# Optimization experiments

Measured on AMD Instinct MI355X. Metric: run time of the kernel, lower is better.

The kernel has to match this reference:

```python
import jax, jax.numpy as jnp
import numpy as np

DIM = 1024
HEADS = 16


def setup_inputs() -> dict:
    key = jax.random.key(0)
    k1, k2, k3, k4 = jax.random.split(key, 4)
    X = jax.random.normal(k1, (4, 2048, DIM), dtype=jnp.float32)
    # torch Linear weight is [out, in]; store transposed [in, out] for x @ W
    W_qkv = jax.random.normal(k2, (DIM, 3 * DIM), dtype=jnp.float32) * (DIM ** -0.5)
    W_out = jax.random.normal(k3, (DIM, DIM), dtype=jnp.float32) * (DIM ** -0.5)
    b_out = jax.random.normal(k4, (DIM,), dtype=jnp.float32) * 0.01
    return {"X": X, "W_qkv": W_qkv, "W_out": W_out, "b_out": b_out}


def reference(X, W_qkv, W_out, b_out):
    b, t, d = X.shape
    h = HEADS
    hd = d // h
    scale = d ** -0.5  # NOTE: scales by full dim, matching the original module
    qkv = X @ W_qkv  # [b, t, 3d]
    q, k, v = jnp.split(qkv, 3, axis=-1)
    # [b, t, d] -> [b, h, t, hd]
    def to_heads(x):
        return x.reshape(b, t, h, hd).transpose(0, 2, 1, 3)
    q, k, v = to_heads(q), to_heads(k), to_heads(v)
    dots = jnp.einsum('bhid,bhjd->bhij', q, k) * scale  # [b, h, t, t]
    attn = jax.nn.softmax(dots, axis=-1)
    out = jnp.einsum('bhij,bhjd->bhid', attn, v)  # [b, h, t, hd]
    out = out.transpose(0, 2, 1, 3).reshape(b, t, d)
    return out @ W_out + b_out
```

## Files before the change

### kernel.cpp

```cpp
#include <hip/hip_runtime.h>
#include <hip/hip_bf16.h>
#include <stdint.h>

#define DIMD 1024
#define NB 4
#define NT 2048
#define NH 16
#define BT (NB*NT)
#define NQKV (3*DIMD)

typedef __attribute__((ext_vector_type(8))) __bf16 bf16x8;
typedef __attribute__((ext_vector_type(4))) __bf16 bf16x4;
typedef __attribute__((ext_vector_type(4))) float f32x4;
typedef __attribute__((ext_vector_type(16))) float f32x16;

#define MFMA16(a,b,c) __builtin_amdgcn_mfma_f32_16x16x32_bf16((a),(b),(c),0,0,0)
#define MFMA32(a,b,c) __builtin_amdgcn_mfma_f32_32x32x16_bf16((a),(b),(c),0,0,0)

#define QSCALE 0.0450842200277801f

__device__ __forceinline__ void gld16(const void* g, void* l) {
  __builtin_amdgcn_global_load_lds((const __attribute__((address_space(1))) void*)g,
                                   (__attribute__((address_space(3))) void*)l,
                                   16, 0, 0);
}

__device__ __forceinline__ unsigned pkbf(float a, float b) {
  unsigned short ua = __builtin_bit_cast(unsigned short, (__bf16)a);
  unsigned short ub = __builtin_bit_cast(unsigned short, (__bf16)b);
  return (unsigned)ua | ((unsigned)ub << 16);
}

__global__ __launch_bounds__(256) void k_cvt(const float* __restrict__ in,
                                             __bf16* __restrict__ out, int n4) {
  int i = blockIdx.x * blockDim.x + threadIdx.x;
  int st = gridDim.x * blockDim.x;
  for (; i < n4; i += st) {
    float4 v = ((const float4*)in)[i];
    bf16x4 o;
    o[0] = (__bf16)v.x; o[1] = (__bf16)v.y; o[2] = (__bf16)v.z; o[3] = (__bf16)v.w;
    ((bf16x4*)out)[i] = o;
  }
}

__global__ __launch_bounds__(256) void k_tcvt(const float* __restrict__ in,
                                              __bf16* __restrict__ out, int K, int N) {
  __shared__ __bf16 t[64][72];
  int n0 = blockIdx.x * 64, k0 = blockIdx.y * 64;
  int r = threadIdx.x >> 2, c0 = (threadIdx.x & 3) * 16;
  const float4* src = (const float4*)(in + (size_t)(k0 + r) * N + n0 + c0);
#pragma unroll
  for (int i = 0; i < 4; ++i) {
    float4 v = src[i];
    t[r][c0 + i*4 + 0] = (__bf16)v.x;
    t[r][c0 + i*4 + 1] = (__bf16)v.y;
    t[r][c0 + i*4 + 2] = (__bf16)v.z;
    t[r][c0 + i*4 + 3] = (__bf16)v.w;
  }
  __syncthreads();
  bf16x8 o0, o1;
#pragma unroll
  for (int i = 0; i < 8; ++i) o0[i] = t[c0 + i][r];
#pragma unroll
  for (int i = 0; i < 8; ++i) o1[i] = t[c0 + 8 + i][r];
  __bf16* dst = out + (size_t)(n0 + r) * K + k0 + c0;
  *(bf16x8*)dst = o0;
  *(bf16x8*)(dst + 8) = o1;
}

template<int MODE>
__global__ __launch_bounds__(512, 1) void k_gemm256(const __bf16* __restrict__ A,
                                                    const __bf16* __restrict__ Bt,
                                                    int nbx,
                                                    __bf16* __restrict__ oQK,
                                                    __bf16* __restrict__ oVt,
                                                    float* __restrict__ oF,
                                                    const float* __restrict__ bias) {
  constexpr int KK = 1024, KT = 32;
  __shared__ alignas(16) char L[98304];
  const int tid = threadIdx.x;
  const int lane = tid & 63, wid = tid >> 6;
  const int lr = lane & 15, lo = lane >> 4;
  const int wm = wid >> 2, wn = wid & 3;
  const int cpx = gridDim.x >> 3;
  const int swz = (blockIdx.x & 7) * cpx + (blockIdx.x >> 3);
  const int bx = swz % nbx, by = swz / nbx;
  const int m0 = by * 128, n0 = bx * 256;

  const int srow = tid >> 2, sk = (tid & 3) * 8;
  const __bf16* Asr = A + (size_t)(m0 + srow) * KK + sk;
  const __bf16* Bs0 = Bt + (size_t)(n0 + srow) * KK + sk;
  const __bf16* Bs1 = Bt + (size_t)(n0 + 128 + srow) * KK + sk;

  auto STAGE = [&](int t) {
    const int s = t & 3;
    char* dA = L + s * 8192 + tid * 16;
    char* dB = L + 32768 + s * 16384 + tid * 16;
    gld16(Asr + t * 32, dA);
    gld16(Bs0 + t * 32, dB);
    gld16(Bs1 + t * 32, dB + 8192);
  };

  const __bf16* fA = (const __bf16*)L + (size_t)(wm * 64 + lr) * 32 + lo * 8;
  const __bf16* fB = (const __bf16*)(L + 32768) + (size_t)(wn * 64 + lr) * 32 + lo * 8;

  f32x4 acc[4][4] = {};
  STAGE(0); STAGE(1); STAGE(2);

  for (int t = 0; t < KT; ++t) {
    if (t < KT - 2)       asm volatile("s_waitcnt vmcnt(6)" ::: "memory");
    else if (t == KT - 2) asm volatile("s_waitcnt vmcnt(3)" ::: "memory");
    else                  asm volatile("s_waitcnt vmcnt(0)" ::: "memory");
    asm volatile("s_barrier" ::: "memory");
    if (t + 3 < KT) STAGE(t + 3);
    const __bf16* fa = fA + (t & 3) * 4096;
    const __bf16* fb = fB + (t & 3) * 8192;
    bf16x8 Af[4], Bf[4];
#pragma unroll
    for (int i = 0; i < 4; ++i) Af[i] = *(const bf16x8*)(fa + i * 512);
#pragma unroll
    for (int j = 0; j < 4; ++j) Bf[j] = *(const bf16x8*)(fb + j * 512);
    __builtin_amdgcn_s_setprio(1);
#pragma unroll
    for (int i = 0; i < 4; ++i)
#pragma unroll
      for (int j = 0; j < 4; ++j)
        acc[i][j] = MFMA16(Af[i], Bf[j], acc[i][j]);
    __builtin_amdgcn_s_setprio(0);
  }

  const int mb = m0 + wm * 64 + lo * 4;
  if (MODE == 0) {
    if (n0 < 1024) {
#pragma unroll
      for (int i = 0; i < 4; ++i)
#pragma unroll
        for (int j = 0; j < 4; ++j) {
          int col = n0 + wn * 64 + j * 16 + lr;
          int row = mb + i * 16;
#pragma unroll
          for (int r = 0; r < 4; ++r)
            oQK[(size_t)(row + r) * 2048 + col] = (__bf16)(acc[i][j][r] * QSCALE);
        }
    } else if (n0 < 2048) {
#pragma unroll
      for (int i = 0; i < 4; ++i)
#pragma unroll
        for (int j = 0; j < 4; ++j) {
          int col = n0 + wn * 64 + j * 16 + lr;
          int row = mb + i * 16;
#pragma unroll
          for (int r = 0; r < 4; ++r)
            oQK[(size_t)(row + r) * 2048 + col] = (__bf16)acc[i][j][r];
        }
    } else {
#pragma unroll
      for (int i = 0; i < 4; ++i)
#pragma unroll
        for (int j = 0; j < 4; ++j) {
          int dd = n0 - 2048 + wn * 64 + j * 16 + lr;
          int row = mb + i * 16;
          int bb = row >> 11, tt = row & 2047;
          bf16x4 pk;
#pragma unroll
          for (int r = 0; r < 4; ++r) pk[r] = (__bf16)acc[i][j][r];
          *(bf16x4*)(oVt + ((size_t)(bb << 10) + dd) * 2048 + tt) = pk;
        }
    }
  } else {
#pragma unroll
    for (int i = 0; i < 4; ++i)
#pragma unroll
      for (int j = 0; j < 4; ++j) {
        int col = n0 + wn * 64 + j * 16 + lr;
        float bv = bias[col];
        int row = mb + i * 16;
#pragma unroll
        for (int r = 0; r < 4; ++r)
          oF[(size_t)(row + r) * 1024 + col] = acc[i][j][r] + bv;
      }
  }
}

__global__ __launch_bounds__(256, 2) void k_attn(const __bf16* __restrict__ QK,
                                                 const __bf16* __restrict__ Vt,
                                                 __bf16* __restrict__ AO) {
  __shared__ alignas(16) __bf16 Ks[2][64 * 72];
  __shared__ alignas(16) __bf16 Vs[2][64 * 72];
  const int tid = threadIdx.x, w = tid >> 6, lane = tid & 63;
  const int l31 = lane & 31, hi = lane >> 5;
  const int P = blockIdx.x;
  const int low3 = P & 7, g = P >> 3;
  const int qc = g & 7;
  const int bh = ((g >> 3) << 3) + low3;
  const int h = bh & 15, b = bh >> 4;
  const int q0 = qc * 256 + w * 64;

  bf16x8 qfA[4], qfB[4];
  {
    const __bf16* Qb = QK + (size_t)(b * 2048 + q0 + l31) * 2048 + h * 64 + hi * 8;
#pragma unroll
    for (int dc = 0; dc < 4; ++dc) qfA[dc] = *(const bf16x8*)(Qb + dc * 16);
    Qb += (size_t)32 * 2048;
#pragma unroll
    for (int dc = 0; dc < 4; ++dc) qfB[dc] = *(const bf16x8*)(Qb + dc * 16);
  }
  const __bf16* Kg = QK + (size_t)(b * 2048) * 2048 + 1024 + h * 64;
  const __bf16* Vg = Vt + (size_t)(b * 1024 + h * 64) * 2048;

  const int i0 = tid, i1 = 256 + tid, i2 = 512 + tid;
  int r0 = i0 / 9, c0 = i0 - r0 * 9; c0 = (c0 == 8) ? 0 : c0;
  int r1 = i1 / 9, c1 = i1 - r1 * 9; c1 = (c1 == 8) ? 0 : c1;
  int r2 = i2 / 9, c2 = i2 - r2 * 9; c2 = (c2 == 8) ? 0 : c2;
  const __bf16* kP0 = Kg + (size_t)r0 * 2048 + c0 * 8;
  const __bf16* kP1 = Kg + (size_t)r1 * 2048 + c1 * 8;
  const __bf16* kP2 = Kg + (size_t)r2 * 2048 + c2 * 8;
  const __bf16* vP0 = Vg + (size_t)r0 * 2048 + c0 * 8;
  const __bf16* vP1 = Vg + (size_t)r1 * 2048 + c1 * 8;
  const __bf16* vP2 = Vg + (size_t)r2 * 2048 + c2 * 8;

  f32x16 oA0 = {0,0,0,0,0,0,0,0,0,0,0,0,0,0,0,0};
  f32x16 oA1 = {0,0,0,0,0,0,0,0,0,0,0,0,0,0,0,0};
  f32x16 oB0 = {0,0,0,0,0,0,0,0,0,0,0,0,0,0,0,0};
  f32x16 oB1 = {0,0,0,0,0,0,0,0,0,0,0,0,0,0,0,0};
  float lnA = 0.f, lnB = 0.f;

  auto STAGE = [&](int x) {
    char* bK = (char*)&Ks[x][0];
    char* bV = (char*)&Vs[x][0];
    gld16(kP0, bK + i0 * 16);
    gld16(vP0, bV + i0 * 16);
    gld16(kP1, bK + i1 * 16);
    gld16(vP1, bV + i1 * 16);
    if (tid < 64) {
      gld16(kP2, bK + i2 * 16);
      gld16(vP2, bV + i2 * 16);
    }
    kP0 += 64 * 2048; kP1 += 64 * 2048; kP2 += 64 * 2048;
    vP0 += 64; vP1 += 64; vP2 += 64;
  };

  auto SMPACK = [&](const f32x16& s0, const f32x16& s1, unsigned pw[4][4], float& ln) {
    float p0a[16], p1a[16];
#pragma unroll
    for (int r = 0; r < 16; ++r) {
      p0a[r] = __builtin_amdgcn_exp2f(s0[r]);
      p1a[r] = __builtin_amdgcn_exp2f(s1[r]);
    }
    float sA = 0.f, sB = 0.f, sC = 0.f, sD = 0.f;
#pragma unroll
    for (int r = 0; r < 4; ++r) {
      sA += p0a[r];      sB += p0a[4 + r];
      sC += p0a[8 + r];  sD += p0a[12 + r];
      sA += p1a[r];      sB += p1a[4 + r];
      sC += p1a[8 + r];  sD += p1a[12 + r];
    }
    ln += (sA + sB) + (sC + sD);
#pragma unroll
    for (int c = 0; c < 4; ++c) {
      const float* pp = (c < 2) ? p0a : p1a;
      const int rb = (c & 1) * 8;
      unsigned A01 = pkbf(pp[rb + 0], pp[rb + 1]);
      unsigned A23 = pkbf(pp[rb + 2], pp[rb + 3]);
      unsigned A45 = pkbf(pp[rb + 4], pp[rb + 5]);
      unsigned A67 = pkbf(pp[rb + 6], pp[rb + 7]);
      asm("v_permlane32_swap_b32 %0, %1" : "+v"(A01), "+v"(A45));
      asm("v_permlane32_swap_b32 %0, %1" : "+v"(A23), "+v"(A67));
      pw[c][0] = A01; pw[c][1] = A23; pw[c][2] = A45; pw[c][3] = A67;
    }
  };

  STAGE(0);
  asm volatile("s_waitcnt vmcnt(0)" ::: "memory");
  __syncthreads();

  int x = 0;
#pragma unroll 2
  for (int t = 0; t < 32; ++t) {
    if (t < 31) STAGE(x ^ 1);
    const __bf16* Kl = &Ks[x][0];
    const __bf16* Vl = &Vs[x][0];

    f32x16 sA0 = {0,0,0,0,0,0,0,0,0,0,0,0,0,0,0,0};
    f32x16 sA1 = {0,0,0,0,0,0,0,0,0,0,0,0,0,0,0,0};
    f32x16 sB0 = {0,0,0,0,0,0,0,0,0,0,0,0,0,0,0,0};
    f32x16 sB1 = {0,0,0,0,0,0,0,0,0,0,0,0,0,0,0,0};
    {
      bf16x8 kf[8];
#pragma unroll
      for (int dc = 0; dc < 4; ++dc)
        kf[dc] = *(const bf16x8*)(Kl + l31 * 72 + dc * 16 + hi * 8);
#pragma unroll
      for (int dc = 0; dc < 4; ++dc)
        kf[4 + dc] = *(const bf16x8*)(Kl + (32 + l31) * 72 + dc * 16 + hi * 8);
      __builtin_amdgcn_s_setprio(1);
#pragma unroll
      for (int dc = 0; dc < 4; ++dc) {
        sA0 = MFMA32(kf[dc], qfA[dc], sA0);
        sB0 = MFMA32(kf[dc], qfB[dc], sB0);
        sA1 = MFMA32(kf[4 + dc], qfA[dc], sA1);
        sB1 = MFMA32(kf[4 + dc], qfB[dc], sB1);
      }
      __builtin_amdgcn_s_setprio(0);
    }

    unsigned pwA[4][4], pwB[4][4];
    SMPACK(sA0, sA1, pwA, lnA);
    SMPACK(sB0, sB1, pwB, lnB);

    {
      bf16x8 vf[8];
#pragma unroll
      for (int c = 0; c < 4; ++c)
        vf[c] = *(const bf16x8*)(Vl + l31 * 72 + c * 16 + hi * 8);
#pragma unroll
      for (int c = 0; c < 4; ++c)
        vf[4 + c] = *(const bf16x8*)(Vl + (32 + l31) * 72 + c * 16 + hi * 8);
      __builtin_amdgcn_s_setprio(1);
#pragma unroll
      for (int c = 0; c < 4; ++c) {
        union { unsigned u[4]; bf16x8 v; } pa, pb;
        pa.u[0] = pwA[c][0]; pa.u[1] = pwA[c][1]; pa.u[2] = pwA[c][2]; pa.u[3] = pwA[c][3];
        pb.u[0] = pwB[c][0]; pb.u[1] = pwB[c][1]; pb.u[2] = pwB[c][2]; pb.u[3] = pwB[c][3];
        oA0 = MFMA32(pa.v, vf[c], oA0);
        oB0 = MFMA32(pb.v, vf[c], oB0);
        oA1 = MFMA32(pa.v, vf[4 + c], oA1);
        oB1 = MFMA32(pb.v, vf[4 + c], oB1);
      }
      __builtin_amdgcn_s_setprio(0);
    }

    asm volatile("s_waitcnt vmcnt(0)" ::: "memory");
    __syncthreads();
    x ^= 1;
  }

  float lA = lnA + __shfl_xor(lnA, 32, 64);
  float lB = lnB + __shfl_xor(lnB, 32, 64);
  float invA = 1.0f / lA, invB = 1.0f / lB;
  __bf16* Ob = AO + (size_t)(b * 2048 + q0) * 1024 + h * 64;
#pragma unroll
  for (int r = 0; r < 16; ++r) {
    int qr = (r & 3) + 8 * (r >> 2) + 4 * hi;
    float ivA = __shfl(invA, qr, 64);
    float ivB = __shfl(invB, qr, 64);
    Ob[(size_t)qr * 1024 + l31] = (__bf16)(oA0[r] * ivA);
    Ob[(size_t)qr * 1024 + 32 + l31] = (__bf16)(oA1[r] * ivA);
    Ob[(size_t)(32 + qr) * 1024 + l31] = (__bf16)(oB0[r] * ivB);
    Ob[(size_t)(32 + qr) * 1024 + 32 + l31] = (__bf16)(oB1[r] * ivB);
  }
}

extern "C" void kernel_launch(void* const* d_in, const int* in_sizes, int n_in,
                              void* d_out, int out_size, void* d_ws, size_t ws_size,
                              hipStream_t stream) {
  const float* X    = (const float*)d_in[0];
  const float* Wqkv = (const float*)d_in[1];
  const float* Wout = (const float*)d_in[2];
  const float* bout = (const float*)d_in[3];
  float* out = (float*)d_out;
  char* ws = (char*)d_ws;

  __bf16* Xb  = (__bf16*)(ws);
  __bf16* Wqt = (__bf16*)(ws + 16777216);
  __bf16* Wot = (__bf16*)(ws + 23068672);
  __bf16* QKb = (__bf16*)(ws + 25165824);
  __bf16* Vtb = (__bf16*)(ws + 58720256);
  __bf16* AOb = (__bf16*)(ws + 75497472);

  k_cvt<<<2048, 256, 0, stream>>>(X, Xb, (BT * DIMD) / 4);
  k_tcvt<<<dim3(NQKV / 64, DIMD / 64), 256, 0, stream>>>(Wqkv, Wqt, DIMD, NQKV);
  k_tcvt<<<dim3(DIMD / 64, DIMD / 64), 256, 0, stream>>>(Wout, Wot, DIMD, DIMD);
  k_gemm256<0><<<768, 512, 0, stream>>>(Xb, Wqt, 12, QKb, Vtb, nullptr, nullptr);
  k_attn<<<512, 256, 0, stream>>>(QKb, Vtb, AOb);
  k_gemm256<1><<<256, 512, 0, stream>>>(AOb, Wot, 4, nullptr, nullptr, out, bout);
}
```

Baseline: 204.1 us.

## Triple-buffer K/V tiles in attention with partial vmcnt waits

Replaces the double-buffered K/V LDS tiles with a three-stage ring buffer. It prefetches two tiles ahead and waits only on the older loads using a partial vmcnt count before a single barrier per iteration. The K/V load assignment is also rebalanced so each thread issues four or five 16-byte async copies, in place of a K/V pair plus an extra for 64 threads. This aims to hide global-load latency better and remove one barrier per iteration. In exchange it uses more LDS per block (about 55KB), which may limit the two-blocks-per-CU occupancy, and it relies on correct vmcnt counting across the ring.

```diff
diff --git a/kernel.cpp b/kernel.cpp
--- a/kernel.cpp
+++ b/kernel.cpp
@@ -185,8 +185,7 @@
 __global__ __launch_bounds__(256, 2) void k_attn(const __bf16* __restrict__ QK,
                                                  const __bf16* __restrict__ Vt,
                                                  __bf16* __restrict__ AO) {
-  __shared__ alignas(16) __bf16 Ks[2][64 * 72];
-  __shared__ alignas(16) __bf16 Vs[2][64 * 72];
+  __shared__ alignas(16) char Lsm[3 * 18432];
   const int tid = threadIdx.x, w = tid >> 6, lane = tid & 63;
   const int l31 = lane & 31, hi = lane >> 5;
   const int P = blockIdx.x;
@@ -208,16 +207,22 @@
   const __bf16* Kg = QK + (size_t)(b * 2048) * 2048 + 1024 + h * 64;
   const __bf16* Vg = Vt + (size_t)(b * 1024 + h * 64) * 2048;
 
-  const int i0 = tid, i1 = 256 + tid, i2 = 512 + tid;
-  int r0 = i0 / 9, c0 = i0 - r0 * 9; c0 = (c0 == 8) ? 0 : c0;
-  int r1 = i1 / 9, c1 = i1 - r1 * 9; c1 = (c1 == 8) ? 0 : c1;
-  int r2 = i2 / 9, c2 = i2 - r2 * 9; c2 = (c2 == 8) ? 0 : c2;
-  const __bf16* kP0 = Kg + (size_t)r0 * 2048 + c0 * 8;
-  const __bf16* kP1 = Kg + (size_t)r1 * 2048 + c1 * 8;
-  const __bf16* kP2 = Kg + (size_t)r2 * 2048 + c2 * 8;
-  const __bf16* vP0 = Vg + (size_t)r0 * 2048 + c0 * 8;
-  const __bf16* vP1 = Vg + (size_t)r1 * 2048 + c1 * 8;
-  const __bf16* vP2 = Vg + (size_t)r2 * 2048 + c2 * 8;
+  const bool nch5 = (tid < 128);
+  const char* gp[5];
+  int loff[5], advB[5];
+#pragma unroll
+  for (int j = 0; j < 5; ++j) {
+    int c = (j < 4) ? (j * 256 + tid) : (1024 + tid);
+    if (c > 1151) c = 1151;
+    int isV = (c >= 576);
+    int lc = isV ? c - 576 : c;
+    int row = lc / 9, col = lc - row * 9; if (col == 8) col = 0;
+    const __bf16* gsrc = isV ? (Vg + (size_t)row * 2048 + col * 8)
+                             : (Kg + (size_t)row * 2048 + col * 8);
+    gp[j] = (const char*)gsrc;
+    loff[j] = c * 16;
+    advB[j] = isV ? 128 : 262144;
+  }
 
   f32x16 oA0 = {0,0,0,0,0,0,0,0,0,0,0,0,0,0,0,0};
   f32x16 oA1 = {0,0,0,0,0,0,0,0,0,0,0,0,0,0,0,0};
@@ -225,19 +230,13 @@
   f32x16 oB1 = {0,0,0,0,0,0,0,0,0,0,0,0,0,0,0,0};
   float lnA = 0.f, lnB = 0.f;
 
-  auto STAGE = [&](int x) {
-    char* bK = (char*)&Ks[x][0];
-    char* bV = (char*)&Vs[x][0];
-    gld16(kP0, bK + i0 * 16);
-    gld16(vP0, bV + i0 * 16);
-    gld16(kP1, bK + i1 * 16);
-    gld16(vP1, bV + i1 * 16);
-    if (tid < 64) {
-      gld16(kP2, bK + i2 * 16);
-      gld16(vP2, bV + i2 * 16);
-    }
-    kP0 += 64 * 2048; kP1 += 64 * 2048; kP2 += 64 * 2048;
-    vP0 += 64; vP1 += 64; vP2 += 64;
+  auto STAGE = [&](int s) {
+    char* bas = Lsm + s * 18432;
+    gld16(gp[0], bas + loff[0]); gp[0] += advB[0];
+    gld16(gp[1], bas + loff[1]); gp[1] += advB[1];
+    gld16(gp[2], bas + loff[2]); gp[2] += advB[2];
+    gld16(gp[3], bas + loff[3]); gp[3] += advB[3];
+    if (nch5) { gld16(gp[4], bas + loff[4]); gp[4] += advB[4]; }
   };
 
   auto SMPACK = [&](const f32x16& s0, const f32x16& s1, unsigned pw[4][4], float& ln) {
@@ -270,16 +269,18 @@
     }
   };
 
-  STAGE(0);
-  asm volatile("s_waitcnt vmcnt(0)" ::: "memory");
-  __syncthreads();
-
-  int x = 0;
-#pragma unroll 2
+  STAGE(0); STAGE(1);
+  int xc = 0, xs = 2;
+
   for (int t = 0; t < 32; ++t) {
-    if (t < 31) STAGE(x ^ 1);
-    const __bf16* Kl = &Ks[x][0];
-    const __bf16* Vl = &Vs[x][0];
+    if (t == 31)   asm volatile("s_waitcnt vmcnt(0)" ::: "memory");
+    else if (nch5) asm volatile("s_waitcnt vmcnt(5)" ::: "memory");
+    else           asm volatile("s_waitcnt vmcnt(4)" ::: "memory");
+    __builtin_amdgcn_s_barrier();
+    if (t <= 29) { STAGE(xs); xs = (xs == 2) ? 0 : xs + 1; }
+
+    const __bf16* Kl = (const __bf16*)(Lsm + xc * 18432);
+    const __bf16* Vl = Kl + 4608;
 
     f32x16 sA0 = {0,0,0,0,0,0,0,0,0,0,0,0,0,0,0,0};
     f32x16 sA1 = {0,0,0,0,0,0,0,0,0,0,0,0,0,0,0,0};
@@ -330,9 +331,7 @@
       __builtin_amdgcn_s_setprio(0);
     }
 
-    asm volatile("s_waitcnt vmcnt(0)" ::: "memory");
-    __syncthreads();
-    x ^= 1;
+    xc = (xc == 2) ? 0 : xc + 1;
   }
 
   float lA = lnA + __shfl_xor(lnA, 32, 64);
```

New measurement: 199.0 us. 1.03x faster.
